# Kernel optimization log

Measured on AMD Instinct MI355X. Metric: run time of the kernel, lower is better.

Reference implementation:

```python
import jax, jax.numpy as jnp
import numpy as np
import math

L, E, H, F, V, ML, B, S = 6, 1024, 16, 4096, 1024, 1024, 4, 1024
PAD = V - 1


def setup_inputs() -> dict:
    key = jax.random.key(0)
    ks = jax.random.split(key, 16)
    sc = 0.02
    nrm = lambda k, sh: jax.random.normal(k, sh, jnp.float32) * sc
    return dict(
        sequences=jax.random.randint(ks[0], (B, S), 0, V - 1),
        embed=nrm(ks[1], (V, E)),
        pos_emb=nrm(ks[2], (1, ML + 2, E)),
        dist_emb=nrm(ks[3], (ML + 1, H)),
        in_w=nrm(ks[4], (L, 3 * E, E)), in_b=nrm(ks[5], (L, 3 * E)),
        out_w=nrm(ks[6], (L, E, E)), out_b=nrm(ks[7], (L, E)),
        ln1_g=jnp.ones((L, E)), ln1_b=jnp.zeros((L, E)),
        ff1_w=nrm(ks[8], (L, F, E)), ff1_b=nrm(ks[9], (L, F)),
        ff2_w=nrm(ks[10], (L, E, F)), ff2_b=nrm(ks[11], (L, E)),
        ln2_g=jnp.ones((L, E)), ln2_b=jnp.zeros((L, E)),
        lnf_g=jnp.ones((E,)), lnf_b=jnp.zeros((E,)),
        gen_w=nrm(ks[12], (V, E)), gen_b=jnp.zeros((V,)),
    )


def _layer_norm(h, g, b, eps=1e-5):
    m = h.mean(-1, keepdims=True)
    v = ((h - m) ** 2).mean(-1, keepdims=True)
    return (h - m) * jax.lax.rsqrt(v + eps) * g + b


def reference(sequences, embed, pos_emb, dist_emb, in_w, in_b, out_w, out_b,
              ln1_g, ln1_b, ff1_w, ff1_b, ff2_w, ff2_b, ln2_g, ln2_b,
              lnf_g, lnf_b, gen_w, gen_b):
    b_, s_ = sequences.shape
    dh = E // H
    # token embedding * sqrt(E) + learned positional embedding
    x = embed[sequences] * math.sqrt(E) + pos_emb[:, :s_]  # [B,S,E]
    # relative-distance attention bias, clamped at max_len
    idx = jnp.arange(s_)
    dist = jnp.minimum(jnp.abs(idx[None, :] - idx[:, None]), ML)  # [S,S]
    bias = dist_emb[dist].transpose(2, 0, 1)[None]  # [1,H,S,S]
    causal = idx[None, :] <= idx[:, None]  # lower-triangular allowed
    bias = jnp.where(causal[None, None], bias, -jnp.inf)
    # key padding mask (additive -inf on padded keys)
    kpm = (sequences == PAD)  # [B,S]
    bias = jnp.where(kpm[:, None, None, :], -jnp.inf, bias)  # [B,H,S,S]

    scale = 1.0 / math.sqrt(dh)
    for l in range(L):
        qkv = jnp.einsum('bse,fe->bsf', x, in_w[l]) + in_b[l]
        q, k, v = jnp.split(qkv, 3, axis=-1)
        q = q.reshape(b_, s_, H, dh).transpose(0, 2, 1, 3)
        k = k.reshape(b_, s_, H, dh).transpose(0, 2, 1, 3)
        v = v.reshape(b_, s_, H, dh).transpose(0, 2, 1, 3)
        scores = jnp.einsum('bhqd,bhkd->bhqk', q, k) * scale + bias
        att = jax.nn.softmax(scores, axis=-1)
        ctx = jnp.einsum('bhqk,bhkd->bhqd', att, v)
        ctx = ctx.transpose(0, 2, 1, 3).reshape(b_, s_, E)
        attn_out = jnp.einsum('bse,fe->bsf', ctx, out_w[l]) + out_b[l]
        x = _layer_norm(x + attn_out, ln1_g[l], ln1_b[l])  # post-norm
        h = jax.nn.gelu(jnp.einsum('bse,fe->bsf', x, ff1_w[l]) + ff1_b[l], approximate=False)
        h = jnp.einsum('bsf,ef->bse', h, ff2_w[l]) + ff2_b[l]
        x = _layer_norm(x + h, ln2_g[l], ln2_b[l])
    x = _layer_norm(x, lnf_g, lnf_b)  # final encoder norm
    logits = jnp.einsum('bse,ve->bsv', x, gen_w) + gen_b
    return logits
```

## Files before the change

### kernel.cpp

```cpp
#include <hip/hip_runtime.h>
#include <math.h>
#include <stdint.h>

constexpr int kL = 6;
constexpr int kE = 1024;
constexpr int kH = 16;
constexpr int kF = 4096;
constexpr int kV = 1024;
constexpr int kB = 4;
constexpr int kS = 1024;
constexpr int kRows = kB * kS;

typedef __bf16 bf16_t;
typedef __bf16 bf16x8 __attribute__((ext_vector_type(8)));
typedef __bf16 bf16x4 __attribute__((ext_vector_type(4)));
typedef float f32x4 __attribute__((ext_vector_type(4)));
typedef unsigned int u32x2 __attribute__((ext_vector_type(2)));

#define AS1 __attribute__((address_space(1)))
#define AS3 __attribute__((address_space(3)))

__device__ __forceinline__ void gload_lds16(const void* g, void* l) {
  __builtin_amdgcn_global_load_lds((const AS1 unsigned int*)g, (AS3 unsigned int*)l, 16, 0, 0);
}

__device__ __forceinline__ unsigned lds_u32(const void* p) {
  return (unsigned)(uintptr_t)p;
}

__device__ __forceinline__ float gelu_f(float x) {
  return 0.5f * x * (1.0f + erff(x * 0.70710678118654752440f));
}

template <int CTRL>
__device__ __forceinline__ float dppf(float v) {
  return __builtin_bit_cast(float, __builtin_amdgcn_update_dpp(
      __builtin_bit_cast(int, v), __builtin_bit_cast(int, v), CTRL, 0xF, 0xF, false));
}

__global__ void cast_kernel(const float* __restrict__ in, bf16_t* __restrict__ out, int n4) {
  const int stride = gridDim.x * blockDim.x;
  for (int i = blockIdx.x * blockDim.x + threadIdx.x; i < n4; i += stride) {
    const float4 v = *(const float4*)(in + (size_t)i * 4);
    bf16x4 o;
    o[0] = (bf16_t)v.x; o[1] = (bf16_t)v.y; o[2] = (bf16_t)v.z; o[3] = (bf16_t)v.w;
    *(bf16x4*)(out + (size_t)i * 4) = o;
  }
}

__global__ void embed_kernel(const int* __restrict__ seq, const float* __restrict__ emb,
                             const float* __restrict__ pos, float* __restrict__ x32,
                             bf16_t* __restrict__ xb) {
  const int r = blockIdx.x;
  const int s = r & 1023;
  const int tok = seq[r];
  const int c = threadIdx.x << 2;
  const float4 e = *(const float4*)(emb + (size_t)tok * kE + c);
  const float4 pz = *(const float4*)(pos + (size_t)s * kE + c);
  float4 v;
  v.x = e.x * 32.0f + pz.x;
  v.y = e.y * 32.0f + pz.y;
  v.z = e.z * 32.0f + pz.z;
  v.w = e.w * 32.0f + pz.w;
  *(float4*)(x32 + (size_t)r * kE + c) = v;
  bf16x4 o;
  o[0] = (bf16_t)v.x; o[1] = (bf16_t)v.y; o[2] = (bf16_t)v.z; o[3] = (bf16_t)v.w;
  *(bf16x4*)(xb + (size_t)r * kE + c) = o;
}

template <int MODE>
__global__ void addln_kernel(float* __restrict__ x32, const void* __restrict__ res,
                             const float* __restrict__ gg, const float* __restrict__ bb,
                             bf16_t* __restrict__ xb, const float* __restrict__ bias2) {
  __shared__ float red[8];
  const int r = blockIdx.x;
  const int c = threadIdx.x << 2;
  float4 v = *(const float4*)(x32 + (size_t)r * kE + c);
  if (MODE == 0) {
    const bf16x4 t = *(const bf16x4*)((const bf16_t*)res + (size_t)r * kE + c);
    v.x += (float)t[0]; v.y += (float)t[1]; v.z += (float)t[2]; v.w += (float)t[3];
  }
  if (MODE == 2) {
    const bf16_t* p = (const bf16_t*)res;
#pragma unroll
    for (int part = 0; part < 4; ++part) {
      const bf16x4 t = *(const bf16x4*)(p + (size_t)part * kRows * kE + (size_t)r * kE + c);
      v.x += (float)t[0]; v.y += (float)t[1]; v.z += (float)t[2]; v.w += (float)t[3];
    }
    const float4 b2 = *(const float4*)(bias2 + c);
    v.x += b2.x; v.y += b2.y; v.z += b2.z; v.w += b2.w;
  }
  float s = v.x + v.y + v.z + v.w;
  float q = v.x * v.x + v.y * v.y + v.z * v.z + v.w * v.w;
#pragma unroll
  for (int off = 32; off >= 1; off >>= 1) {
    s += __shfl_xor(s, off, 64);
    q += __shfl_xor(q, off, 64);
  }
  const int w = threadIdx.x >> 6, lane = threadIdx.x & 63;
  if (lane == 0) { red[w] = s; red[4 + w] = q; }
  __syncthreads();
  s = red[0] + red[1] + red[2] + red[3];
  q = red[4] + red[5] + red[6] + red[7];
  const float mean = s * (1.0f / 1024.0f);
  const float var = q * (1.0f / 1024.0f) - mean * mean;
  const float rstd = rsqrtf(var + 1e-5f);
  const float4 g4 = *(const float4*)(gg + c);
  const float4 b4 = *(const float4*)(bb + c);
  float4 o;
  o.x = (v.x - mean) * rstd * g4.x + b4.x;
  o.y = (v.y - mean) * rstd * g4.y + b4.y;
  o.z = (v.z - mean) * rstd * g4.z + b4.z;
  o.w = (v.w - mean) * rstd * g4.w + b4.w;
  if (MODE != 1) *(float4*)(x32 + (size_t)r * kE + c) = o;
  bf16x4 ob;
  ob[0] = (bf16_t)o.x; ob[1] = (bf16_t)o.y; ob[2] = (bf16_t)o.z; ob[3] = (bf16_t)o.w;
  *(bf16x4*)(xb + (size_t)r * kE + c) = ob;
}

template <int EPI>
__launch_bounds__(256, 4)
__global__ void gemm128_kernel(const bf16_t* __restrict__ A, const bf16_t* __restrict__ Bt,
                               const float* __restrict__ bias, void* __restrict__ Cv,
                               int ldA, int ldB, int ldC, int kc, size_t zstride) {
  __shared__ bf16_t lA[64 * 64];
  __shared__ bf16_t lB[64 * 64];
  const int tid = threadIdx.x;
  const int w = tid >> 6;
  const int lane = tid & 63;
  const int g = lane >> 4;
  const int lr = lane & 15;

  const int nwg = gridDim.x * gridDim.y;
  const int lin = blockIdx.y * gridDim.x + blockIdx.x;
  const int cpx = nwg >> 3;
  const int swz = (lin & 7) * cpx + (lin >> 3);
  const int bx = swz % gridDim.x, by = swz / gridDim.x;
  const int bm0 = by << 7;
  const int bn0 = bx << 7;
  const int k0 = blockIdx.z * kc;
  const int wm = (w >> 1) << 6;
  const int wn = (w & 1) << 6;

  const int ln8 = lane >> 3, l8 = lane & 7;
  const int pg = l8 ^ ln8;
  const int arow0 = (w << 5) + (ln8 << 1) + (pg >> 2);
  const int arow1 = arow0 + 16;
  const int kpo = (pg & 3) << 3;
  const bf16_t* srcA0 = A + (size_t)(bm0 + arow0) * ldA + k0 + kpo;
  const bf16_t* srcA1 = A + (size_t)(bm0 + arow1) * ldA + k0 + kpo;
  const bf16_t* srcB0 = Bt + (size_t)(bn0 + arow0) * ldB + k0 + kpo;
  const bf16_t* srcB1 = Bt + (size_t)(bn0 + arow1) * ldB + k0 + kpo;
  bf16_t* dA0 = lA + (w << 10);
  bf16_t* dA1 = lA + (w << 10) + 512;
  bf16_t* dB0 = lB + (w << 10);
  bf16_t* dB1 = lB + (w << 10) + 512;

  f32x4 zz = {0.f, 0.f, 0.f, 0.f};
  f32x4 acc[4][4];
#pragma unroll
  for (int i = 0; i < 4; ++i)
#pragma unroll
    for (int j = 0; j < 4; ++j) acc[i][j] = zz;

  int paoff[4], pboff[4];
#pragma unroll
  for (int i = 0; i < 4; ++i) {
    const int ra = wm + i * 16 + lr;
    paoff[i] = ((ra >> 1) << 6) + (((((ra & 1) << 2) + g) ^ ((ra >> 1) & 7)) << 3);
    const int rb = wn + i * 16 + lr;
    pboff[i] = ((rb >> 1) << 6) + (((((rb & 1) << 2) + g) ^ ((rb >> 1) & 7)) << 3);
  }

  const int NT = kc >> 5;
  for (int t = 0; t < NT; ++t) {
    gload_lds16(srcA0, dA0);
    gload_lds16(srcA1, dA1);
    gload_lds16(srcB0, dB0);
    gload_lds16(srcB1, dB1);
    srcA0 += 32; srcA1 += 32; srcB0 += 32; srcB1 += 32;
    __syncthreads();
    bf16x8 a[4], b[4];
#pragma unroll
    for (int i = 0; i < 4; ++i) a[i] = *(const bf16x8*)&lA[paoff[i]];
#pragma unroll
    for (int i = 0; i < 4; ++i) b[i] = *(const bf16x8*)&lB[pboff[i]];
#pragma unroll
    for (int i = 0; i < 4; ++i)
#pragma unroll
      for (int j = 0; j < 4; ++j)
        acc[i][j] = __builtin_amdgcn_mfma_f32_16x16x32_bf16(a[i], b[j], acc[i][j], 0, 0, 0);
    __syncthreads();
  }

  bf16_t* outb = (bf16_t*)Cv;
  if (EPI == 3) outb += (size_t)blockIdx.z * zstride;
#pragma unroll
  for (int i = 0; i < 4; ++i) {
#pragma unroll
    for (int j = 0; j < 4; ++j) {
      const int col = bn0 + wn + j * 16 + lr;
      float bv = 0.0f;
      if (EPI != 3) bv = bias[col];
#pragma unroll
      for (int rg = 0; rg < 4; ++rg) {
        const int row = bm0 + wm + i * 16 + g * 4 + rg;
        float v = acc[i][j][rg] + bv;
        if (EPI == 2) v = gelu_f(v);
        if (EPI == 1) {
          ((float*)Cv)[(size_t)row * ldC + col] = v;
        } else {
          outb[(size_t)row * ldC + col] = (bf16_t)v;
        }
      }
    }
  }
}

__launch_bounds__(256, 3)
__global__ void attn_kernel(const bf16_t* __restrict__ qkv, const int* __restrict__ seq,
                            const float* __restrict__ dist_emb, bf16_t* __restrict__ ctx) {
  __shared__ float sbias[1024];
  __shared__ unsigned char spad[1024];
  __shared__ bf16_t kbuf[2][64 * 64];
  __shared__ bf16_t vbuf[2][4096];
  __shared__ bf16_t pbuf[4][16][72];
  const int tid = threadIdx.x;
  const int w = tid >> 6, lane = tid & 63, g = lane >> 4, lr = lane & 15;
  const int bid = blockIdx.x;
  const int qt = 15 - (bid >> 6);
  const int h = bid & 15, b = (bid >> 4) & 3;

  const int q0 = qt * 64 + w * 16;
  const bf16_t* qp = qkv + ((size_t)(b * kS + q0 + lr)) * 3072 + h * 64;

  const int p = (w * 64 + lane) * 16;
  const int s_kv = ((p >> 11) << 4) + ((p >> 5) & 15);
  const int s_dv = (((p >> 9) & 3) << 4) + ((p & 31) >> 1);
  const bf16_t* vsrc0 = qkv + ((size_t)(b * kS + s_kv)) * 3072 + 2048 + h * 64 + s_dv;

  const int klrow = (w << 3) + (lane >> 3);
  const int kscol = ((lane & 7) ^ (lane >> 3)) << 3;
  const bf16_t* ksrc0 = qkv + ((size_t)(b * kS + klrow)) * 3072 + 1024 + h * 64 + kscol;

  const int cs0k = (g ^ (lr & 7)) << 3;
  const int cs1k = ((4 + g) ^ (lr & 7)) << 3;

  const int* seqb = seq + b * kS;
  const int nt = qt + 1;

#define STAGEKV(bufi, kt_) {                                                        \
    gload_lds16(ksrc0 + (size_t)((kt_) * 64) * 3072, &kbuf[bufi][(w << 3) * 64]);   \
    gload_lds16(ksrc0 + (size_t)((kt_) * 64 + 32) * 3072,                           \
                &kbuf[bufi][(32 + (w << 3)) * 64]);                                 \
    gload_lds16(vsrc0 + (size_t)((kt_) * 64) * 3072, &vbuf[bufi][w << 9]);          \
    gload_lds16(vsrc0 + (size_t)((kt_) * 64 + 32) * 3072,                           \
                &vbuf[bufi][2048 + (w << 9)]);                                      \
  }

  STAGEKV(0, 0);
  const bf16x8 qf0 = *(const bf16x8*)(qp + g * 8);
  const bf16x8 qf1 = *(const bf16x8*)(qp + 32 + g * 8);
  for (int i = tid; i < 1024; i += 256) {
    sbias[i] = dist_emb[i * kH + h];
    spad[i] = (seqb[i] == kV - 1) ? 1 : 0;
  }

  f32x4 zz = {0.f, 0.f, 0.f, 0.f};
  f32x4 oacc[4];
#pragma unroll
  for (int n = 0; n < 4; ++n) oacc[n] = zz;
  float m_[4], l_[4];
#pragma unroll
  for (int j = 0; j < 4; ++j) { m_[j] = -1e30f; l_[j] = 0.f; }

  __syncthreads();

#define ATT_STEP64(kt_, bz) do {                                                    \
    bf16x8 kf0[4], kf1[4];                                                          \
    _Pragma("unroll")                                                               \
    for (int ns = 0; ns < 4; ++ns) {                                                \
      const int krow = (ns * 16 + lr) * 64;                                         \
      kf0[ns] = *(const bf16x8*)&kbuf[bz][krow + cs0k];                             \
      kf1[ns] = *(const bf16x8*)&kbuf[bz][krow + cs1k];                             \
    }                                                                               \
    f32x4 s_[4];                                                                    \
    _Pragma("unroll")                                                               \
    for (int ns = 0; ns < 4; ++ns) {                                                \
      f32x4 z = zz;                                                                 \
      z = __builtin_amdgcn_mfma_f32_16x16x32_bf16(qf0, kf0[ns], z, 0, 0, 0);        \
      z = __builtin_amdgcn_mfma_f32_16x16x32_bf16(qf1, kf1[ns], z, 0, 0, 0);        \
      s_[ns] = z;                                                                   \
    }                                                                               \
    const int colb = (kt_) * 64 + lr;                                               \
    bool pad[4];                                                                    \
    _Pragma("unroll")                                                               \
    for (int ns = 0; ns < 4; ++ns) pad[ns] = spad[colb + ns * 16] != 0;             \
    float sv[4][4], mj[4];                                                          \
    _Pragma("unroll")                                                               \
    for (int j = 0; j < 4; ++j) {                                                   \
      const int r = q0 + g * 4 + j;                                                 \
      _Pragma("unroll")                                                             \
      for (int ns = 0; ns < 4; ++ns) {                                              \
        const int cc = colb + ns * 16;                                              \
        sv[ns][j] = (cc <= r && !pad[ns]) ? s_[ns][j] * 0.125f + sbias[r - cc]      \
                                          : -1e30f;                                 \
      }                                                                             \
      mj[j] = fmaxf(fmaxf(sv[0][j], sv[1][j]), fmaxf(sv[2][j], sv[3][j]));          \
      mj[j] = fmaxf(mj[j], dppf<0x121>(mj[j]));                                     \
      mj[j] = fmaxf(mj[j], dppf<0x122>(mj[j]));                                     \
      mj[j] = fmaxf(mj[j], dppf<0x124>(mj[j]));                                     \
      mj[j] = fmaxf(mj[j], dppf<0x128>(mj[j]));                                     \
    }                                                                               \
    float corr[4], pv[4][4];                                                        \
    _Pragma("unroll")                                                               \
    for (int j = 0; j < 4; ++j) {                                                   \
      const float mn = fmaxf(m_[j], mj[j]);                                         \
      corr[j] = __expf(m_[j] - mn);                                                 \
      m_[j] = mn;                                                                   \
      _Pragma("unroll")                                                             \
      for (int ns = 0; ns < 4; ++ns) pv[ns][j] = __expf(sv[ns][j] - mn);            \
      float rs = (pv[0][j] + pv[1][j]) + (pv[2][j] + pv[3][j]);                     \
      rs += dppf<0x121>(rs);                                                        \
      rs += dppf<0x122>(rs);                                                        \
      rs += dppf<0x124>(rs);                                                        \
      rs += dppf<0x128>(rs);                                                        \
      l_[j] = l_[j] * corr[j] + rs;                                                 \
    }                                                                               \
    _Pragma("unroll")                                                               \
    for (int n = 0; n < 4; ++n) {                                                   \
      f32x4 t = oacc[n];                                                            \
      t[0] *= corr[0]; t[1] *= corr[1]; t[2] *= corr[2]; t[3] *= corr[3];           \
      oacc[n] = t;                                                                  \
    }                                                                               \
    _Pragma("unroll")                                                               \
    for (int j = 0; j < 4; ++j) {                                                   \
      _Pragma("unroll")                                                             \
      for (int ns = 0; ns < 4; ++ns)                                                \
        pbuf[w][g * 4 + j][ns * 16 + lr] = (bf16_t)pv[ns][j];                       \
    }                                                                               \
    asm volatile("s_waitcnt lgkmcnt(0)" ::: "memory");                              \
    const bf16x4 pa0 = *(const bf16x4*)&pbuf[w][lr][g * 4];                         \
    const bf16x4 pa1 = *(const bf16x4*)&pbuf[w][lr][16 + g * 4];                    \
    const bf16x4 pa2 = *(const bf16x4*)&pbuf[w][lr][32 + g * 4];                    \
    const bf16x4 pa3 = *(const bf16x4*)&pbuf[w][lr][48 + g * 4];                    \
    bf16x8 pfl, pfh;                                                                \
    _Pragma("unroll")                                                               \
    for (int j = 0; j < 4; ++j) {                                                   \
      pfl[j] = pa0[j]; pfl[4 + j] = pa1[j];                                         \
      pfh[j] = pa2[j]; pfh[4 + j] = pa3[j];                                         \
    }                                                                               \
    const unsigned vb0 = lds_u32(&vbuf[bz][0]) + g * 128 + lr * 8;                  \
    u32x2 vt[8], vth[8];                                                            \
    _Pragma("unroll")                                                               \
    for (int n = 0; n < 4; ++n) {                                                   \
      asm volatile("ds_read_b64_tr_b16 %0, %2\n\t"                                  \
                   "ds_read_b64_tr_b16 %1, %2 offset:2048"                          \
                   : "=&v"(vt[n * 2]), "=&v"(vt[n * 2 + 1])                         \
                   : "v"(vb0 + n * 512)                                             \
                   : "memory");                                                     \
      asm volatile("ds_read_b64_tr_b16 %0, %2 offset:4096\n\t"                      \
                   "ds_read_b64_tr_b16 %1, %2 offset:6144"                          \
                   : "=&v"(vth[n * 2]), "=&v"(vth[n * 2 + 1])                       \
                   : "v"(vb0 + n * 512)                                             \
                   : "memory");                                                     \
    }                                                                               \
    asm volatile("s_waitcnt lgkmcnt(0)" ::: "memory");                              \
    __builtin_amdgcn_sched_barrier(0);                                              \
    _Pragma("unroll")                                                               \
    for (int n = 0; n < 4; ++n) {                                                   \
      const bf16x4 v0 = __builtin_bit_cast(bf16x4, vt[n * 2]);                      \
      const bf16x4 v1 = __builtin_bit_cast(bf16x4, vt[n * 2 + 1]);                  \
      bf16x8 vf;                                                                    \
      _Pragma("unroll")                                                             \
      for (int j = 0; j < 4; ++j) { vf[j] = v0[j]; vf[4 + j] = v1[j]; }             \
      oacc[n] = __builtin_amdgcn_mfma_f32_16x16x32_bf16(pfl, vf, oacc[n], 0, 0, 0); \
      const bf16x4 h0 = __builtin_bit_cast(bf16x4, vth[n * 2]);                     \
      const bf16x4 h1 = __builtin_bit_cast(bf16x4, vth[n * 2 + 1]);                 \
      bf16x8 vfh;                                                                   \
      _Pragma("unroll")                                                             \
      for (int j = 0; j < 4; ++j) { vfh[j] = h0[j]; vfh[4 + j] = h1[j]; }           \
      oacc[n] = __builtin_amdgcn_mfma_f32_16x16x32_bf16(pfh, vfh, oacc[n], 0, 0, 0);\
    }                                                                               \
  } while (0)

  for (int kt = 0; kt < nt; kt += 2) {
    if (kt + 1 < nt) STAGEKV(1, kt + 1);
    ATT_STEP64(kt, 0);
    __syncthreads();
    if (kt + 2 < nt) STAGEKV(0, kt + 2);
    if (kt + 1 < nt) ATT_STEP64(kt + 1, 1);
    __syncthreads();
  }
#undef ATT_STEP64
#undef STAGEKV

#pragma unroll
  for (int j = 0; j < 4; ++j) {
    const float inv = 1.0f / l_[j];
    const int r = q0 + g * 4 + j;
    bf16_t* dst = ctx + ((size_t)(b * kS + r)) * kE + h * 64;
#pragma unroll
    for (int n = 0; n < 4; ++n) dst[n * 16 + lr] = (bf16_t)(oacc[n][j] * inv);
  }
}

extern "C" void kernel_launch(void* const* d_in, const int* in_sizes, int n_in,
                              void* d_out, int out_size, void* d_ws, size_t ws_size,
                              hipStream_t stream) {
  (void)in_sizes; (void)n_in; (void)out_size;
  const int* seq = (const int*)d_in[0];
  const float* emb = (const float*)d_in[1];
  const float* pos = (const float*)d_in[2];
  const float* dist = (const float*)d_in[3];
  const float* in_w = (const float*)d_in[4];
  const float* in_b = (const float*)d_in[5];
  const float* out_w = (const float*)d_in[6];
  const float* out_b = (const float*)d_in[7];
  const float* ln1g = (const float*)d_in[8];
  const float* ln1b = (const float*)d_in[9];
  const float* ff1w = (const float*)d_in[10];
  const float* ff1b = (const float*)d_in[11];
  const float* ff2w = (const float*)d_in[12];
  const float* ff2b = (const float*)d_in[13];
  const float* ln2g = (const float*)d_in[14];
  const float* ln2b = (const float*)d_in[15];
  const float* lnfg = (const float*)d_in[16];
  const float* lnfb = (const float*)d_in[17];
  const float* genw = (const float*)d_in[18];
  const float* genb = (const float*)d_in[19];

  char* ws = (char*)d_ws;
  size_t off = 0;
  auto alloc = [&](size_t elems, size_t esz) -> void* {
    void* pp = ws + off;
    off += (elems * esz + 255) & ~(size_t)255;
    return pp;
  };
  bf16_t* w_in = (bf16_t*)alloc((size_t)kL * 3 * kE * kE, 2);
  bf16_t* w_out = (bf16_t*)alloc((size_t)kL * kE * kE, 2);
  bf16_t* w_f1 = (bf16_t*)alloc((size_t)kL * kF * kE, 2);
  bf16_t* w_f2 = (bf16_t*)alloc((size_t)kL * kE * kF, 2);
  bf16_t* w_g = (bf16_t*)alloc((size_t)kV * kE, 2);
  float* x32 = (float*)alloc((size_t)kRows * kE, 4);
  bf16_t* xb = (bf16_t*)alloc((size_t)kRows * kE, 2);
  bf16_t* qkvb = (bf16_t*)alloc((size_t)kRows * 3 * kE, 2);
  bf16_t* ctxb = (bf16_t*)alloc((size_t)kRows * kE, 2);
  bf16_t* tmp4 = (bf16_t*)alloc((size_t)4 * kRows * kE, 2);
  bf16_t* hb = (bf16_t*)alloc((size_t)kRows * kF, 2);
  if (off > ws_size) return;

  cast_kernel<<<2048, 256, 0, stream>>>(in_w, w_in, kL * 3 * kE * kE / 4);
  cast_kernel<<<2048, 256, 0, stream>>>(out_w, w_out, kL * kE * kE / 4);
  cast_kernel<<<2048, 256, 0, stream>>>(ff1w, w_f1, kL * kF * kE / 4);
  cast_kernel<<<2048, 256, 0, stream>>>(ff2w, w_f2, kL * kE * kF / 4);
  cast_kernel<<<1024, 256, 0, stream>>>(genw, w_g, kV * kE / 4);
  embed_kernel<<<kRows, 256, 0, stream>>>(seq, emb, pos, x32, xb);

  for (int l = 0; l < kL; ++l) {
    gemm128_kernel<0><<<dim3(3 * kE / 128, kRows / 128), 256, 0, stream>>>(
        xb, w_in + (size_t)l * 3 * kE * kE, in_b + (size_t)l * 3 * kE, qkvb,
        kE, kE, 3 * kE, kE, 0);
    attn_kernel<<<kB * kH * 16, 256, 0, stream>>>(qkvb, seq, dist, ctxb);
    gemm128_kernel<3><<<dim3(kE / 128, kRows / 128, 4), 256, 0, stream>>>(
        ctxb, w_out + (size_t)l * kE * kE, nullptr, tmp4,
        kE, kE, kE, 256, (size_t)kRows * kE);
    addln_kernel<2><<<kRows, 256, 0, stream>>>(x32, tmp4, ln1g + (size_t)l * kE,
                                               ln1b + (size_t)l * kE, xb, out_b + (size_t)l * kE);
    gemm128_kernel<2><<<dim3(kF / 128, kRows / 128), 256, 0, stream>>>(
        xb, w_f1 + (size_t)l * kF * kE, ff1b + (size_t)l * kF, hb,
        kE, kE, kF, kE, 0);
    gemm128_kernel<3><<<dim3(kE / 128, kRows / 128, 4), 256, 0, stream>>>(
        hb, w_f2 + (size_t)l * kE * kF, nullptr, tmp4,
        kF, kF, kE, kE, (size_t)kRows * kE);
    addln_kernel<2><<<kRows, 256, 0, stream>>>(x32, tmp4, ln2g + (size_t)l * kE,
                                               ln2b + (size_t)l * kE, xb, ff2b + (size_t)l * kE);
  }
  addln_kernel<1><<<kRows, 256, 0, stream>>>(x32, nullptr, lnfg, lnfb, xb, nullptr);
  gemm128_kernel<1><<<dim3(kV / 128, kRows / 128), 256, 0, stream>>>(
      xb, w_g, genb, (float*)d_out, kE, kE, kV, kE, 0);
}
```

Measured before the change: 1.405 ms.

## Double-buffer LDS tiles in gemm128 to overlap global loads with MFMA

Splits the 128x128 GEMM kernel's shared-memory tiles into two buffers and prefetches the next K-slice into the alternate buffer while the current one feeds the MFMAs. Partial vmcnt waits plus raw barriers replace the full __syncthreads pair. The goal is to hide global-to-LDS latency that was previously exposed on every iteration. In exchange, LDS use per block doubles, which could reduce occupancy under the (256,4) launch bounds.

```diff
diff --git a/kernel.cpp b/kernel.cpp
--- a/kernel.cpp
+++ b/kernel.cpp
@@ -123,8 +123,8 @@
 __global__ void gemm128_kernel(const bf16_t* __restrict__ A, const bf16_t* __restrict__ Bt,
                                const float* __restrict__ bias, void* __restrict__ Cv,
                                int ldA, int ldB, int ldC, int kc, size_t zstride) {
-  __shared__ bf16_t lA[64 * 64];
-  __shared__ bf16_t lB[64 * 64];
+  __shared__ bf16_t lA[2][64 * 64];
+  __shared__ bf16_t lB[2][64 * 64];
   const int tid = threadIdx.x;
   const int w = tid >> 6;
   const int lane = tid & 63;
@@ -151,10 +151,7 @@
   const bf16_t* srcA1 = A + (size_t)(bm0 + arow1) * ldA + k0 + kpo;
   const bf16_t* srcB0 = Bt + (size_t)(bn0 + arow0) * ldB + k0 + kpo;
   const bf16_t* srcB1 = Bt + (size_t)(bn0 + arow1) * ldB + k0 + kpo;
-  bf16_t* dA0 = lA + (w << 10);
-  bf16_t* dA1 = lA + (w << 10) + 512;
-  bf16_t* dB0 = lB + (w << 10);
-  bf16_t* dB1 = lB + (w << 10) + 512;
+  const int dO = w << 10;
 
   f32x4 zz = {0.f, 0.f, 0.f, 0.f};
   f32x4 acc[4][4];
@@ -172,26 +169,42 @@
     pboff[i] = ((rb >> 1) << 6) + (((((rb & 1) << 2) + g) ^ ((rb >> 1) & 7)) << 3);
   }
 
+#define STAGE128(bufi, t) {                                           \
+    gload_lds16(srcA0 + (size_t)(t) * 32, &lA[bufi][dO]);             \
+    gload_lds16(srcA1 + (size_t)(t) * 32, &lA[bufi][dO + 512]);       \
+    gload_lds16(srcB0 + (size_t)(t) * 32, &lB[bufi][dO]);             \
+    gload_lds16(srcB1 + (size_t)(t) * 32, &lB[bufi][dO + 512]);       \
+  }
+
   const int NT = kc >> 5;
+  STAGE128(0, 0);
   for (int t = 0; t < NT; ++t) {
-    gload_lds16(srcA0, dA0);
-    gload_lds16(srcA1, dA1);
-    gload_lds16(srcB0, dB0);
-    gload_lds16(srcB1, dB1);
-    srcA0 += 32; srcA1 += 32; srcB0 += 32; srcB1 += 32;
-    __syncthreads();
+    const int bz = t & 1;
+    if (t + 1 < NT) {
+      STAGE128(bz ^ 1, t + 1);
+      __builtin_amdgcn_sched_barrier(0);
+      asm volatile("s_waitcnt vmcnt(4)" ::: "memory");
+    } else {
+      __builtin_amdgcn_sched_barrier(0);
+      asm volatile("s_waitcnt vmcnt(0)" ::: "memory");
+    }
+    __builtin_amdgcn_s_barrier();
+    __builtin_amdgcn_sched_barrier(0);
     bf16x8 a[4], b[4];
 #pragma unroll
-    for (int i = 0; i < 4; ++i) a[i] = *(const bf16x8*)&lA[paoff[i]];
-#pragma unroll
-    for (int i = 0; i < 4; ++i) b[i] = *(const bf16x8*)&lB[pboff[i]];
+    for (int i = 0; i < 4; ++i) a[i] = *(const bf16x8*)&lA[bz][paoff[i]];
+#pragma unroll
+    for (int i = 0; i < 4; ++i) b[i] = *(const bf16x8*)&lB[bz][pboff[i]];
 #pragma unroll
     for (int i = 0; i < 4; ++i)
 #pragma unroll
       for (int j = 0; j < 4; ++j)
         acc[i][j] = __builtin_amdgcn_mfma_f32_16x16x32_bf16(a[i], b[j], acc[i][j], 0, 0, 0);
-    __syncthreads();
-  }
+    __builtin_amdgcn_sched_barrier(0);
+    __builtin_amdgcn_s_barrier();
+    __builtin_amdgcn_sched_barrier(0);
+  }
+#undef STAGE128
 
   bf16_t* outb = (bf16_t*)Cv;
   if (EPI == 3) outb += (size_t)blockIdx.z * zstride;
```

Result: no change. 1.425 ms (+1.4%).
